# Performance work log

Measured on AMD Instinct MI355X. Metric: run time of the kernel, lower is better.

The kernel has to match this reference:

```python
import jax, jax.numpy as jnp
import numpy as np

T, B = 1024, 256
N = T * B
D = 128  # d_model
IN = 36  # lstm input size = 16 + 4 + 16


def _w(k, shape, s=0.1):
    return jax.random.normal(k, shape, dtype=jnp.float32) * s


def setup_inputs() -> dict:
    key = jax.random.key(0)
    ks = jax.random.split(key, 32)
    inp = {}
    inp["image"] = jax.random.uniform(ks[0], (N, 1, 3, 3), jnp.float32) * 255.0
    inp["location"] = jax.random.uniform(ks[1], (N, 2), jnp.float32) * 5.0
    inp["message"] = jax.random.randint(ks[2], (N,), 0, 16)
    inp["done"] = (jax.random.uniform(ks[3], (N,)) < 0.05).astype(jnp.float32)
    inp["h0"] = jax.random.normal(ks[4], (1, B, D), jnp.float32)
    inp["c0"] = jax.random.normal(ks[5], (1, B, D), jnp.float32)
    # visual encoder: 9 -> 256 -> 256 -> 128 -> 16 (ReLU each)
    inp["vis_W1"] = _w(ks[6], (256, 9));   inp["vis_b1"] = jnp.zeros((256,), jnp.float32)
    inp["vis_W2"] = _w(ks[7], (256, 256)); inp["vis_b2"] = jnp.zeros((256,), jnp.float32)
    inp["vis_W3"] = _w(ks[8], (128, 256)); inp["vis_b3"] = jnp.zeros((128,), jnp.float32)
    inp["vis_W4"] = _w(ks[9], (16, 128));  inp["vis_b4"] = jnp.zeros((16,), jnp.float32)
    # location encoder: 2 -> 4
    inp["loc_W"] = _w(ks[10], (4, 2)); inp["loc_b"] = jnp.zeros((4,), jnp.float32)
    # message encoder: Embedding(16,16) -> Linear(16,16) -> ReLU
    inp["emb"] = _w(ks[11], (16, 16), 1.0)
    inp["msg_W"] = _w(ks[12], (16, 16)); inp["msg_b"] = jnp.zeros((16,), jnp.float32)
    # LSTM params (torch layout, gate order i,f,g,o)
    inp["W_ih"] = _w(ks[13], (4 * D, IN)); inp["W_hh"] = _w(ks[14], (4 * D, D))
    inp["b_ih"] = jnp.zeros((4 * D,), jnp.float32); inp["b_hh"] = jnp.zeros((4 * D,), jnp.float32)
    # heads
    inp["actor_W"] = _w(ks[15], (5, D), 0.01);   inp["actor_b"] = jnp.zeros((5,), jnp.float32)
    inp["head_W"] = _w(ks[16], (16, D), 0.01);   inp["head_b"] = jnp.zeros((16,), jnp.float32)
    inp["critic_W"] = _w(ks[17], (1, D), 1.0);   inp["critic_b"] = jnp.zeros((1,), jnp.float32)
    return inp


def reference(image, location, message, done, h0, c0,
              vis_W1, vis_b1, vis_W2, vis_b2, vis_W3, vis_b3, vis_W4, vis_b4,
              loc_W, loc_b, emb, msg_W, msg_b,
              W_ih, W_hh, b_ih, b_hh,
              actor_W, actor_b, head_W, head_b, critic_W, critic_b):
    # encoders (all rows at once)
    x = image.reshape(N, -1) / 255.0
    x = jax.nn.relu(x @ vis_W1.T + vis_b1)
    x = jax.nn.relu(x @ vis_W2.T + vis_b2)
    x = jax.nn.relu(x @ vis_W3.T + vis_b3)
    img_feat = jax.nn.relu(x @ vis_W4.T + vis_b4)                 # [N,16]
    loc_feat = (location / 5.0) @ loc_W.T + loc_b                 # [N,4]
    msg_feat = jax.nn.relu(emb[message] @ msg_W.T + msg_b)        # [N,16]
    feat = jnp.concatenate([img_feat, loc_feat, msg_feat], axis=1).reshape(T, B, IN)
    d = done.reshape(T, B)

    def step(carry, inp_t):
        h, c = carry
        x_t, d_t = inp_t
        m = (1.0 - d_t)[:, None]
        h = h * m
        c = c * m
        gates = x_t @ W_ih.T + h @ W_hh.T + (b_ih + b_hh)         # [B,4D]
        i, f, g, o = jnp.split(gates, 4, axis=-1)
        i = jax.nn.sigmoid(i); f = jax.nn.sigmoid(f)
        g = jnp.tanh(g);       o = jax.nn.sigmoid(o)
        c = f * c + i * g
        h = o * jnp.tanh(c)
        return (h, c), h

    (_, _), hs = jax.lax.scan(step, (h0[0], c0[0]), (feat, d))
    hidden = hs.reshape(N, D)
    action_logits = hidden @ actor_W.T + actor_b                  # [N,5]
    message_logits = hidden @ head_W.T + head_b                   # [N,16]
    value = hidden @ critic_W.T + critic_b                        # [N,1]
    return jnp.concatenate([action_logits, message_logits, value], axis=1)  # [N,22]
```

## Files before the change

kernel.cpp:

```cpp
#include <hip/hip_runtime.h>
#include <hip/hip_bf16.h>

#define DEV __device__ __forceinline__

typedef short short8 __attribute__((ext_vector_type(8)));
typedef _Float16 h8 __attribute__((ext_vector_type(8)));
typedef _Float16 h2 __attribute__((ext_vector_type(2)));
typedef float f32x4 __attribute__((ext_vector_type(4)));
typedef unsigned short u16;

constexpr int T_ = 1024, B_ = 256, N_ = T_ * B_, D_ = 128;
constexpr int FS = 48;
constexpr int NSLOT = 16;
constexpr int SEGQC = 64;
constexpr int MAXIT = 392;
constexpr int CH = 48;
constexpr int WARM = 56;
constexpr int MAXPC = 768;
constexpr unsigned DEADT = 0xFFFFu;
constexpr unsigned TRB = 0x10000u;
constexpr unsigned NWB = 0x20000u;

DEV u16 f2b(float f) {
  unsigned u = __float_as_uint(f);
  return (u16)((u + 0x7fffu + ((u >> 16) & 1u)) >> 16);
}

#if __has_builtin(__builtin_amdgcn_exp2f)
#define EXP2F __builtin_amdgcn_exp2f
#else
#define EXP2F __exp2f
#endif
#if __has_builtin(__builtin_amdgcn_rcpf)
#define RCPF __builtin_amdgcn_rcpf
#else
#define RCPF(x) (1.0f / (x))
#endif
DEV float sigf(float x) { return RCPF(1.0f + EXP2F(x * -1.44269504f)); }
DEV float tanhf_(float x) {
  return fmaf(RCPF(1.0f + EXP2F(x * -2.88539008f)), 2.0f, -1.0f);
}

__global__ void prep_kernel(const float* W1, const float* W2, const float* W3,
                            const float* W4, const float* emb, const float* msgW,
                            const float* msgb, const float* Wih, const float* Whh,
                            const float* bih, const float* bhh, const float* aW,
                            const float* ab, const float* hW, const float* hb,
                            const float* cW, const float* cb, u16* w1p, u16* w2b,
                            u16* w3b, u16* w4b, float* msgtab, _Float16* wfull,
                            float* biass, _Float16* w22, float* b22) {
  int i0 = blockIdx.x * blockDim.x + threadIdx.x;
  int st = gridDim.x * blockDim.x;
  for (int i = i0; i < 256 * 32; i += st) {
    int r = i >> 5, k = i & 31;
    w1p[i] = (k < 9) ? f2b(W1[r * 9 + k]) : (u16)0;
  }
  for (int i = i0; i < 256 * 256; i += st) w2b[i] = f2b(W2[i]);
  for (int i = i0; i < 128 * 256; i += st) w3b[i] = f2b(W3[i]);
  for (int i = i0; i < 16 * 128; i += st) w4b[i] = f2b(W4[i]);
  for (int i = i0; i < 256; i += st) {
    int v = i >> 4, j = i & 15;
    float s = msgb[j];
    for (int k = 0; k < 16; ++k) s += emb[v * 16 + k] * msgW[j * 16 + k];
    msgtab[i] = s > 0.f ? s : 0.f;
  }
  for (int i = i0; i < 512 * 192; i += st) {
    int c = i / 192, k = i % 192;
    float v;
    if (k < 128) v = Whh[(size_t)c * 128 + k];
    else {
      int p = k - 128;
      if (p < 18) v = Wih[(size_t)c * 36 + p];
      else if (p >= 24 && p < 42) v = Wih[(size_t)c * 36 + p - 6];
      else v = 0.f;
    }
    wfull[i] = (_Float16)v;
  }
  for (int i = i0; i < 512; i += st) biass[i] = bih[i] + bhh[i];
  for (int i = i0; i < 32 * 128; i += st) {
    int c = i >> 7, k = i & 127;
    float v = 0.f;
    if (c < 5) v = aW[c * 128 + k];
    else if (c < 21) v = hW[(c - 5) * 128 + k];
    else if (c == 21) v = cW[k];
    w22[i] = (_Float16)v;
  }
  for (int i = i0; i < 32; i += st) {
    float v = 0.f;
    if (i < 5) v = ab[i];
    else if (i < 21) v = hb[i - 5];
    else if (i == 21) v = cb[0];
    b22[i] = v;
  }
}

__global__ __launch_bounds__(64) void seg_scan_kernel(const float* done,
                                                      unsigned* segq, int* nq) {
  __shared__ unsigned short brkpos[1024];
  __shared__ int lcnt[64];
  __shared__ int nb_sh;
  __shared__ int pcs[MAXPC];
  __shared__ int np_sh;
  const int b = blockIdx.x;
  const int l = threadIdx.x;

  unsigned mask = 0;
#pragma unroll
  for (int j = 0; j < 16; ++j) {
    const int t = l * 16 + j;
    const float dv = (t == 0) ? 0.0f : done[(size_t)t * B_ + b];
    mask |= (dv != 0.0f) ? (1u << j) : 0u;
  }
  lcnt[l] = __popc(mask);
  __syncthreads();
  if (l == 0) {
    int acc = 0;
    for (int i = 0; i < 64; ++i) { const int c = lcnt[i]; lcnt[i] = acc; acc += c; }
    nb_sh = acc;
  }
  __syncthreads();
  {
    int off = lcnt[l];
    unsigned mm = mask;
    while (mm) {
      const int j = __builtin_ctz(mm);
      mm &= mm - 1;
      brkpos[off++] = (unsigned short)(l * 16 + j);
    }
  }
  __syncthreads();
  if (l == 0) {
    int np = 0;
    const int nb = nb_sh;
    int t0 = 0;
    for (int s = 0; s <= nb; ++s) {
      const int t1 = (s < nb) ? (int)brkpos[s] : T_;
      int k = 0;
      for (int ps = t0; ps < t1 && np < MAXPC; ps += CH, ++k) {
        const int pl = min(CH, t1 - ps);
        const int wl = (k == 0) ? 0 : min(WARM, ps - t0);
        pcs[np++] = ps | (pl << 10) | (wl << 17);
      }
      t0 = t1;
    }
    np_sh = np;
  }
  __syncthreads();
  const int np = np_sh;
  int ssum[16], scnt[16];
#pragma unroll
  for (int j = 0; j < 16; ++j) { ssum[j] = 0; scnt[j] = 0; }
  if (l == 0 && np > 0) {
    const int e = pcs[0];
    segq[((size_t)b * NSLOT + 0) * SEGQC + 0] = (unsigned)e;
    ssum[0] = ((e >> 10) & 127) + ((e >> 17) & 127);
    scnt[0] = 1;
    pcs[0] = -1;
  }
  __syncthreads();
  for (int it = 1; it < np; ++it) {
    int bestw = -1, bestk = 0;
    for (int j = l; j < np; j += 64) {
      const int e = pcs[j];
      if (e >= 0) {
        const int w = ((e >> 10) & 127) + ((e >> 17) & 127);
        if (w > bestw || (w == bestw && j < bestk)) { bestw = w; bestk = j; }
      }
    }
    int pk = (bestw < 0) ? -1 : ((bestw << 10) | (1023 - bestk));
#pragma unroll
    for (int wd = 32; wd >= 1; wd >>= 1) pk = max(pk, __shfl_xor(pk, wd));
    if (l == 0 && pk >= 0) {
      const int k = 1023 - (pk & 1023);
      const int e = pcs[k];
      const int w = pk >> 10;
      int m = 0, best = 0x7fffffff;
#pragma unroll
      for (int j = 0; j < 16; ++j) {
        const int v = (scnt[j] >= SEGQC) ? 0x7fffffff : ssum[j];
        if (v < best) { best = v; m = j; }
      }
      segq[((size_t)b * NSLOT + m) * SEGQC + scnt[m]] = (unsigned)e;
      ssum[m] += w;
      ++scnt[m];
      pcs[k] = -1;
    }
    __syncthreads();
  }
  if (l == 0) {
#pragma unroll
    for (int j = 0; j < 16; ++j) nq[b * NSLOT + j] = scnt[j];
  }
}

__global__ __launch_bounds__(64) void sched_build_kernel(const unsigned* segq,
                                                         const int* nq,
                                                         unsigned* sched,
                                                         int* bsteps) {
  const int b = blockIdx.x;
  const int l = threadIdx.x;
  int it = 0;
  if (l < NSLOT) {
    const int gs = b * NSLOT + l;
    const unsigned* q = segq + (size_t)gs * SEGQC;
    const int cnt = nq[gs];
    unsigned* sc = sched + (size_t)b * MAXIT * 16 + l;
    for (int s = 0; s < cnt; ++s) {
      const unsigned e = q[s];
      const int ps = (int)(e & 1023u);
      const int pl = (int)((e >> 10) & 127u);
      const int wl = (int)((e >> 17) & 127u);
      for (int j = 0; j < wl && it < MAXIT - 8; ++j) {
        sc[(size_t)it * 16] = (unsigned)(ps - wl + j) | NWB;
        ++it;
      }
      for (int j = 0; j < pl && it < MAXIT - 8; ++j) {
        sc[(size_t)it * 16] = (unsigned)(ps + j) | ((j == pl - 1) ? TRB : 0u);
        ++it;
      }
    }
  }
  int mk = (l < NSLOT) ? it : 0;
#pragma unroll
  for (int w = 8; w >= 1; w >>= 1) mk = max(mk, __shfl_xor(mk, w));
  if (l < NSLOT) {
    unsigned* sc = sched + (size_t)b * MAXIT * 16 + l;
    const int pe = min(mk + 8, MAXIT);
    for (int i2 = it; i2 < pe; ++i2) sc[(size_t)i2 * 16] = DEADT | TRB;
    if (l == 0) bsteps[b] = mk;
  }
}

template <int K, int OUTN, bool SWZIN>
DEV void mlp_layer(const u16* Ain, u16* Aout, const u16* Wb, const float* bias,
                   int colbase, int NT, int lane) {
  constexpr int KT = K / 32;
  const int lr = lane & 15, lg = lane >> 4;
  for (int nt = 0; nt < NT; ++nt) {
    const int col = colbase + nt * 16 + lr;
    short8 bf[KT];
#pragma unroll
    for (int kt = 0; kt < KT; ++kt)
      bf[kt] = *(const short8*)(Wb + col * K + kt * 32 + lg * 8);
    const float bcol = bias[col];
#pragma unroll
    for (int mt = 0; mt < 4; ++mt) {
      f32x4 acc = {0.f, 0.f, 0.f, 0.f};
#pragma unroll
      for (int kt = 0; kt < KT; ++kt) {
        const int row = mt * 16 + lr;
        int kb = (kt * 32 + lg * 8) * 2;
        if (SWZIN) kb ^= (row & 7) << 4;
        const short8 af = *(const short8*)(Ain + row * K + (kb >> 1));
        acc = __builtin_amdgcn_mfma_f32_16x16x32_bf16(af, bf[kt], acc, 0, 0, 0);
      }
#pragma unroll
      for (int r = 0; r < 4; ++r) {
        const int row = mt * 16 + lg * 4 + r;
        float v = acc[r] + bcol;
        v = v > 0.f ? v : 0.f;
        const int kb = (col * 2) ^ ((row & 7) << 4);
        Aout[row * OUTN + (kb >> 1)] = f2b(v);
      }
    }
  }
}

__global__ __launch_bounds__(256) void enc_kernel(
    const float* image, const float* location, const int* message,
    const float* vb1, const float* vb2, const float* vb3, const float* vb4,
    const float* locW, const float* locb, const u16* w1p, const u16* w2b,
    const u16* w3b, const u16* w4b, const float* msgtab, _Float16* featf) {
  __shared__ __align__(16) u16 buf1[64 * 256];
  __shared__ __align__(16) u16 buf2[64 * 256];
  const int n0 = blockIdx.x * 64;
  const int tid = threadIdx.x;
  const int wave = tid >> 6, lane = tid & 63;

  for (int i = tid; i < 64 * 32; i += 256) {
    int r = i >> 5, k = i & 31;
    float v = (k < 9) ? image[(size_t)(n0 + r) * 9 + k] * (1.0f / 255.0f) : 0.0f;
    buf2[i] = f2b(v);
  }
  __syncthreads();
  mlp_layer<32, 256, false>(buf2, buf1, w1p, vb1, wave * 64, 4, lane);
  __syncthreads();
  mlp_layer<256, 256, true>(buf1, buf2, w2b, vb2, wave * 64, 4, lane);
  __syncthreads();
  mlp_layer<256, 128, true>(buf2, buf1, w3b, vb3, wave * 32, 2, lane);
  __syncthreads();
  {
    const int lr = lane & 15, lg = lane >> 4;
    const int col = lr;
    short8 bfr[4];
#pragma unroll
    for (int kt = 0; kt < 4; ++kt)
      bfr[kt] = *(const short8*)(w4b + col * 128 + kt * 32 + lg * 8);
    f32x4 acc = {0.f, 0.f, 0.f, 0.f};
#pragma unroll
    for (int kt = 0; kt < 4; ++kt) {
      const int row = wave * 16 + lr;
      const int kb = ((kt * 32 + lg * 8) * 2) ^ ((row & 7) << 4);
      const short8 af = *(const short8*)(buf1 + row * 128 + (kb >> 1));
      acc = __builtin_amdgcn_mfma_f32_16x16x32_bf16(af, bfr[kt], acc, 0, 0, 0);
    }
    const float bcol = vb4[col];
#pragma unroll
    for (int r = 0; r < 4; ++r) {
      const int row = wave * 16 + lg * 4 + r;
      float v = acc[r] + bcol;
      v = v > 0.f ? v : 0.f;
      featf[(size_t)(n0 + row) * FS + col] = (_Float16)v;
    }
  }
  if (tid < 64) {
    const int n = n0 + tid;
    _Float16* fr = featf + (size_t)n * FS;
#pragma unroll
    for (int j = 0; j < 6; ++j) fr[18 + j] = (_Float16)0.f;
#pragma unroll
    for (int j = 0; j < 6; ++j) fr[42 + j] = (_Float16)0.f;
    const float x0 = location[(size_t)n * 2] * 0.2f;
    const float x1 = location[(size_t)n * 2 + 1] * 0.2f;
#pragma unroll
    for (int j = 0; j < 4; ++j) {
      const int pos = (j < 2) ? 16 + j : 22 + j;
      fr[pos] = (_Float16)fmaf(x0, locW[j * 2], fmaf(x1, locW[j * 2 + 1], locb[j]));
    }
    const float* mrow = msgtab + message[n] * 16;
#pragma unroll
    for (int j = 0; j < 16; ++j) fr[26 + j] = (_Float16)mrow[j];
  }
}

__global__ __launch_bounds__(512, 2) void lstm_seg_kernel(
    const _Float16* featf, const _Float16* wfull, const float* biass,
    const unsigned* sched, const int* bsteps, const float* h0, const float* c0,
    const float* done, _Float16* hidh) {
  __shared__ __align__(16) char abuf[2][16 * 384];
  const int b = blockIdx.x;
  const int tid = threadIdx.x;
  const int wave = tid >> 6, l = tid & 63;
  const int lc = l & 15, lg = l >> 4;
  const int d = wave * 16 + lc;
  const bool fth = (wave < 6) && (lc < 4);
  const int fslot = lg * 4 + lc;
  const int fch = wave;

  h8 bf[4][6];
#pragma unroll
  for (int g = 0; g < 4; ++g) {
    const _Float16* wp = wfull + (size_t)(g * 128 + d) * 192;
#pragma unroll
    for (int kt = 0; kt < 6; ++kt)
      bf[g][kt] = *(const h8*)(wp + kt * 32 + lg * 8);
  }
  float bias4[4];
#pragma unroll
  for (int g = 0; g < 4; ++g) bias4[g] = biass[g * 128 + d];

  for (int i = tid; i < 2 * 16 * 384 / 4; i += 512) ((float*)abuf)[i] = 0.0f;
  __syncthreads();

  const int nsteps = bsteps[b];
  const unsigned* sb = sched + (size_t)b * MAXIT * 16;
  uint4 sr0 = *(const uint4*)(sb + 0 * 16 + lg * 4);
  uint4 sr1 = *(const uint4*)(sb + 1 * 16 + lg * 4);
  unsigned ss1 = DEADT, ss2 = DEADT, t00 = DEADT;
  if (fth) {
    t00 = sb[0 * 16 + fslot] & 0xFFFFu;
    ss1 = sb[1 * 16 + fslot];
    ss2 = sb[2 * 16 + fslot];
  }

  const float m0 = 1.0f - done[b];
  if (tid < 128)
    *(_Float16*)(abuf[0] + 2 * tid) = (_Float16)(h0[(size_t)b * D_ + tid] * m0);
  float creg[4];
#pragma unroll
  for (int r = 0; r < 4; ++r) {
    const int row = lg * 4 + r;
    creg[r] = (row == 0) ? c0[(size_t)b * D_ + d] * m0 : 0.0f;
  }
  if (fth && t00 != DEADT) {
    const unsigned fo = t00 * (unsigned)(B_ * FS) + (unsigned)(b * FS) + fch * 8;
    const uint4 fz = *(const uint4*)(featf + fo);
    const int byte = (fslot * 384 + 256 + fch * 16) ^ ((fslot & 7) << 4);
    *(uint4*)(abuf[0] + byte) = fz;
  }
  uint4 fvW = {0, 0, 0, 0};
  if (fth && (ss1 & 0xFFFFu) != DEADT) {
    const unsigned fo =
        (ss1 & 0xFFFFu) * (unsigned)(B_ * FS) + (unsigned)(b * FS) + fch * 8;
    fvW = *(const uint4*)(featf + fo);
  }
  __syncthreads();

  int p = 0;
  for (int i = 0; i < nsteps; ++i) {
    const uint4 srN = *(const uint4*)(sb + (size_t)(i + 2) * 16 + lg * 4);
    unsigned ssN = DEADT;
    if (fth) ssN = sb[(size_t)(i + 3) * 16 + fslot];
    const char* bp = abuf[p];
    h8 af[6];
#pragma unroll
    for (int kt = 0; kt < 6; ++kt) {
      const int byte = (lc * 384 + ((kt * 32 + lg * 8) << 1)) ^ ((lc & 7) << 4);
      af[kt] = *(const h8*)(bp + byte);
    }
    uint4 fvN = {0, 0, 0, 0};
    const unsigned t2 = ss2 & 0xFFFFu;
    if (fth && t2 != DEADT) {
      const unsigned fo = t2 * (unsigned)(B_ * FS) + (unsigned)(b * FS) + fch * 8;
      fvN = *(const uint4*)(featf + fo);
    }
    f32x4 acc[4];
#pragma unroll
    for (int g = 0; g < 4; ++g)
      acc[g] = f32x4{bias4[g], bias4[g], bias4[g], bias4[g]};
#pragma unroll
    for (int kt = 0; kt < 6; ++kt)
#pragma unroll
      for (int g = 0; g < 4; ++g)
        acc[g] = __builtin_amdgcn_mfma_f32_16x16x32_f16(af[kt], bf[g][kt],
                                                        acc[g], 0, 0, 0);
    char* bn = abuf[p ^ 1];
#pragma unroll
    for (int r = 0; r < 4; ++r) {
      const int row = lg * 4 + r;
      const unsigned e = ((const unsigned*)&sr0)[r];
      const float gi = sigf(acc[0][r]);
      const float gf = sigf(acc[1][r]);
      const float gg = tanhf_(acc[2][r]);
      const float go = sigf(acc[3][r]);
      const float cn = fmaf(gf, creg[r], gi * gg);
      const float hv = go * tanhf_(cn);
      const unsigned tt = e & 0xFFFFu;
      const bool tr = (e & TRB) != 0u;
      creg[r] = tr ? 0.0f : cn;
      *(_Float16*)(bn + ((row * 384 + 2 * d) ^ ((row & 7) << 4))) =
          (_Float16)(tr ? 0.0f : hv);
      if (tt != DEADT && !(e & NWB)) {
        const unsigned ho = (tt << 15) + (unsigned)((b << 7) + d);
        hidh[ho] = (_Float16)hv;
      }
    }
    if (fth && (ss1 & 0xFFFFu) != DEADT) {
      const int byte = (fslot * 384 + 256 + fch * 16) ^ ((fslot & 7) << 4);
      *(uint4*)(bn + byte) = fvW;
    }
    sr0 = sr1; sr1 = srN;
    ss1 = ss2; ss2 = ssN;
    fvW = fvN;
    asm volatile("s_waitcnt lgkmcnt(0)" ::: "memory");
    __builtin_amdgcn_s_barrier();
    p ^= 1;
  }
}

__global__ __launch_bounds__(256) void head_kernel(const _Float16* hidh,
                                                   const _Float16* w22,
                                                   const float* b22, float* out) {
  const int tid = threadIdx.x;
  const int w = tid >> 6, l = tid & 63;
  const int lr = l & 15, lg = l >> 4;
  const int row0 = blockIdx.x * 64 + w * 16;

  h8 bfr[2][4];
#pragma unroll
  for (int ct = 0; ct < 2; ++ct)
#pragma unroll
    for (int kt = 0; kt < 4; ++kt)
      bfr[ct][kt] = *(const h8*)(w22 + (ct * 16 + lr) * 128 + kt * 32 + lg * 8);
  h8 af[4];
#pragma unroll
  for (int kt = 0; kt < 4; ++kt)
    af[kt] = *(const h8*)(hidh + (size_t)(row0 + lr) * D_ + kt * 32 + lg * 8);

  f32x4 acc[2];
#pragma unroll
  for (int ct = 0; ct < 2; ++ct) acc[ct] = f32x4{0.f, 0.f, 0.f, 0.f};
#pragma unroll
  for (int kt = 0; kt < 4; ++kt)
#pragma unroll
    for (int ct = 0; ct < 2; ++ct)
      acc[ct] = __builtin_amdgcn_mfma_f32_16x16x32_f16(af[kt], bfr[ct][kt],
                                                       acc[ct], 0, 0, 0);
#pragma unroll
  for (int ct = 0; ct < 2; ++ct) {
    const int col = ct * 16 + lr;
    if (col < 22) {
      const float bb = b22[col];
#pragma unroll
      for (int r = 0; r < 4; ++r) {
        const int row = row0 + lg * 4 + r;
        out[(size_t)row * 22 + col] = acc[ct][r] + bb;
      }
    }
  }
}

extern "C" void kernel_launch(void* const* d_in, const int* in_sizes, int n_in,
                              void* d_out, int out_size, void* d_ws, size_t ws_size,
                              hipStream_t stream) {
  const float* image = (const float*)d_in[0];
  const float* location = (const float*)d_in[1];
  const int* message = (const int*)d_in[2];
  const float* done = (const float*)d_in[3];
  const float* h0 = (const float*)d_in[4];
  const float* c0 = (const float*)d_in[5];
  const float* vW1 = (const float*)d_in[6];
  const float* vb1 = (const float*)d_in[7];
  const float* vW2 = (const float*)d_in[8];
  const float* vb2 = (const float*)d_in[9];
  const float* vW3 = (const float*)d_in[10];
  const float* vb3 = (const float*)d_in[11];
  const float* vW4 = (const float*)d_in[12];
  const float* vb4 = (const float*)d_in[13];
  const float* locW = (const float*)d_in[14];
  const float* locb = (const float*)d_in[15];
  const float* emb = (const float*)d_in[16];
  const float* msgW = (const float*)d_in[17];
  const float* msgb = (const float*)d_in[18];
  const float* Wih = (const float*)d_in[19];
  const float* Whh = (const float*)d_in[20];
  const float* bih = (const float*)d_in[21];
  const float* bhh = (const float*)d_in[22];
  const float* aW = (const float*)d_in[23];
  const float* ab = (const float*)d_in[24];
  const float* hW = (const float*)d_in[25];
  const float* hb = (const float*)d_in[26];
  const float* cW = (const float*)d_in[27];
  const float* cb = (const float*)d_in[28];

  char* ws = (char*)d_ws;
  size_t off = 0;
  auto alloc = [&](size_t bytes) {
    void* p = ws + off;
    off = (off + bytes + 255) & ~(size_t)255;
    return p;
  };
  _Float16* featf = (_Float16*)alloc((size_t)N_ * FS * 2);
  _Float16* hidh = (_Float16*)alloc((size_t)N_ * D_ * 2);
  u16* w1p = (u16*)alloc(256 * 32 * 2);
  u16* w2b = (u16*)alloc(256 * 256 * 2);
  u16* w3b = (u16*)alloc(128 * 256 * 2);
  u16* w4b = (u16*)alloc(16 * 128 * 2);
  float* msgtab = (float*)alloc(256 * 4);
  _Float16* wfull = (_Float16*)alloc(512 * 192 * 2);
  float* biass = (float*)alloc(512 * 4);
  unsigned* segq = (unsigned*)alloc((size_t)B_ * NSLOT * SEGQC * 4);
  int* nqA = (int*)alloc(B_ * NSLOT * 4);
  unsigned* sched = (unsigned*)alloc((size_t)B_ * MAXIT * 16 * 4);
  int* bsteps = (int*)alloc(B_ * 4);
  _Float16* w22 = (_Float16*)alloc(32 * 128 * 2);
  float* b22 = (float*)alloc(32 * 4);
  (void)in_sizes; (void)n_in; (void)out_size; (void)ws_size;

  prep_kernel<<<64, 256, 0, stream>>>(vW1, vW2, vW3, vW4, emb, msgW, msgb, Wih,
                                      Whh, bih, bhh, aW, ab, hW, hb, cW, cb, w1p,
                                      w2b, w3b, w4b, msgtab, wfull, biass, w22,
                                      b22);
  seg_scan_kernel<<<B_, 64, 0, stream>>>(done, segq, nqA);
  sched_build_kernel<<<B_, 64, 0, stream>>>(segq, nqA, sched, bsteps);
  enc_kernel<<<N_ / 64, 256, 0, stream>>>(image, location, message, vb1, vb2, vb3,
                                          vb4, locW, locb, w1p, w2b, w3b, w4b,
                                          msgtab, featf);
  lstm_seg_kernel<<<B_, 512, 0, stream>>>(featf, wfull, biass, sched, bsteps,
                                          h0, c0, done, hidh);
  head_kernel<<<N_ / 64, 256, 0, stream>>>(hidh, w22, b22, (float*)d_out);
}
```

Before: 481.0 us.

## Enlarge encoder tile to 128 rows with 2x4 wave grid and register-blocked MFMA

The encoder kernel now handles 128 rows per block with 8 waves arranged as 2 row-halves by 4 column-quarters. Each wave loads its A fragments once per row tile and reuses them across two output column tiles, and the accumulators are seeded with the bias. This cuts repeated LDS reads and weight loads per output and should expose more MFMA ILP. The cost is 128KB of LDS per block, which lowers occupancy to one block per CU. The prep kernel grid is also doubled.

```diff
diff --git a/kernel.cpp b/kernel.cpp
--- a/kernel.cpp
+++ b/kernel.cpp
@@ -232,88 +232,110 @@
 }
 
 template <int K, int OUTN, bool SWZIN>
-DEV void mlp_layer(const u16* Ain, u16* Aout, const u16* Wb, const float* bias,
-                   int colbase, int NT, int lane) {
+DEV void mlp_layer128(const u16* Ain, u16* Aout, const u16* Wb, const float* bias,
+                      int mh, int cq, int lane) {
   constexpr int KT = K / 32;
+  constexpr int NT = OUTN / 64;
+  constexpr int PASSES = NT / 2;
   const int lr = lane & 15, lg = lane >> 4;
-  for (int nt = 0; nt < NT; ++nt) {
-    const int col = colbase + nt * 16 + lr;
-    short8 bf[KT];
-#pragma unroll
-    for (int kt = 0; kt < KT; ++kt)
-      bf[kt] = *(const short8*)(Wb + col * K + kt * 32 + lg * 8);
-    const float bcol = bias[col];
+  const int colbase = cq * (OUTN / 4);
+  const int rowbase = mh * 64;
+#pragma unroll
+  for (int ps = 0; ps < PASSES; ++ps) {
+    short8 bf[2][KT];
+    float bcol[2];
+#pragma unroll
+    for (int n2 = 0; n2 < 2; ++n2) {
+      const int col = colbase + (ps * 2 + n2) * 16 + lr;
+#pragma unroll
+      for (int kt = 0; kt < KT; ++kt)
+        bf[n2][kt] = *(const short8*)(Wb + col * K + kt * 32 + lg * 8);
+      bcol[n2] = bias[col];
+    }
 #pragma unroll
     for (int mt = 0; mt < 4; ++mt) {
-      f32x4 acc = {0.f, 0.f, 0.f, 0.f};
+      const int arow = rowbase + mt * 16 + lr;
+      short8 af[KT];
 #pragma unroll
       for (int kt = 0; kt < KT; ++kt) {
-        const int row = mt * 16 + lr;
         int kb = (kt * 32 + lg * 8) * 2;
-        if (SWZIN) kb ^= (row & 7) << 4;
-        const short8 af = *(const short8*)(Ain + row * K + (kb >> 1));
-        acc = __builtin_amdgcn_mfma_f32_16x16x32_bf16(af, bf[kt], acc, 0, 0, 0);
-      }
-#pragma unroll
-      for (int r = 0; r < 4; ++r) {
-        const int row = mt * 16 + lg * 4 + r;
-        float v = acc[r] + bcol;
-        v = v > 0.f ? v : 0.f;
-        const int kb = (col * 2) ^ ((row & 7) << 4);
-        Aout[row * OUTN + (kb >> 1)] = f2b(v);
-      }
-    }
-  }
-}
-
-__global__ __launch_bounds__(256) void enc_kernel(
+        if (SWZIN) kb ^= (arow & 7) << 4;
+        af[kt] = *(const short8*)(Ain + arow * K + (kb >> 1));
+      }
+      f32x4 acc[2];
+#pragma unroll
+      for (int n2 = 0; n2 < 2; ++n2)
+        acc[n2] = f32x4{bcol[n2], bcol[n2], bcol[n2], bcol[n2]};
+#pragma unroll
+      for (int kt = 0; kt < KT; ++kt)
+#pragma unroll
+        for (int n2 = 0; n2 < 2; ++n2)
+          acc[n2] = __builtin_amdgcn_mfma_f32_16x16x32_bf16(af[kt], bf[n2][kt],
+                                                            acc[n2], 0, 0, 0);
+#pragma unroll
+      for (int n2 = 0; n2 < 2; ++n2) {
+        const int col = colbase + (ps * 2 + n2) * 16 + lr;
+#pragma unroll
+        for (int r = 0; r < 4; ++r) {
+          const int orow = rowbase + mt * 16 + lg * 4 + r;
+          float v = acc[n2][r];
+          v = v > 0.f ? v : 0.f;
+          const int kb = (col * 2) ^ ((orow & 7) << 4);
+          Aout[orow * OUTN + (kb >> 1)] = f2b(v);
+        }
+      }
+    }
+  }
+}
+
+__global__ __launch_bounds__(512) void enc_kernel(
     const float* image, const float* location, const int* message,
     const float* vb1, const float* vb2, const float* vb3, const float* vb4,
     const float* locW, const float* locb, const u16* w1p, const u16* w2b,
     const u16* w3b, const u16* w4b, const float* msgtab, _Float16* featf) {
-  __shared__ __align__(16) u16 buf1[64 * 256];
-  __shared__ __align__(16) u16 buf2[64 * 256];
-  const int n0 = blockIdx.x * 64;
+  __shared__ __align__(16) u16 bufA[128 * 256];
+  __shared__ __align__(16) u16 bufB[128 * 256];
+  const int n0 = blockIdx.x * 128;
   const int tid = threadIdx.x;
   const int wave = tid >> 6, lane = tid & 63;
-
-  for (int i = tid; i < 64 * 32; i += 256) {
+  const int mh = wave >> 2, cq = wave & 3;
+
+  for (int i = tid; i < 128 * 32; i += 512) {
     int r = i >> 5, k = i & 31;
     float v = (k < 9) ? image[(size_t)(n0 + r) * 9 + k] * (1.0f / 255.0f) : 0.0f;
-    buf2[i] = f2b(v);
-  }
-  __syncthreads();
-  mlp_layer<32, 256, false>(buf2, buf1, w1p, vb1, wave * 64, 4, lane);
-  __syncthreads();
-  mlp_layer<256, 256, true>(buf1, buf2, w2b, vb2, wave * 64, 4, lane);
-  __syncthreads();
-  mlp_layer<256, 128, true>(buf2, buf1, w3b, vb3, wave * 32, 2, lane);
+    bufA[i] = f2b(v);
+  }
+  __syncthreads();
+  mlp_layer128<32, 256, false>(bufA, bufB, w1p, vb1, mh, cq, lane);
+  __syncthreads();
+  mlp_layer128<256, 256, true>(bufB, bufA, w2b, vb2, mh, cq, lane);
+  __syncthreads();
+  mlp_layer128<256, 128, true>(bufA, bufB, w3b, vb3, mh, cq, lane);
   __syncthreads();
   {
     const int lr = lane & 15, lg = lane >> 4;
-    const int col = lr;
     short8 bfr[4];
 #pragma unroll
     for (int kt = 0; kt < 4; ++kt)
-      bfr[kt] = *(const short8*)(w4b + col * 128 + kt * 32 + lg * 8);
-    f32x4 acc = {0.f, 0.f, 0.f, 0.f};
+      bfr[kt] = *(const short8*)(w4b + lr * 128 + kt * 32 + lg * 8);
+    const float bcol = vb4[lr];
+    f32x4 acc = {bcol, bcol, bcol, bcol};
 #pragma unroll
     for (int kt = 0; kt < 4; ++kt) {
-      const int row = wave * 16 + lr;
-      const int kb = ((kt * 32 + lg * 8) * 2) ^ ((row & 7) << 4);
-      const short8 af = *(const short8*)(buf1 + row * 128 + (kb >> 1));
+      const int arow = wave * 16 + lr;
+      const int kb = ((kt * 32 + lg * 8) * 2) ^ ((arow & 7) << 4);
+      const short8 af = *(const short8*)(bufB + arow * 128 + (kb >> 1));
       acc = __builtin_amdgcn_mfma_f32_16x16x32_bf16(af, bfr[kt], acc, 0, 0, 0);
     }
-    const float bcol = vb4[col];
 #pragma unroll
     for (int r = 0; r < 4; ++r) {
       const int row = wave * 16 + lg * 4 + r;
-      float v = acc[r] + bcol;
+      float v = acc[r];
       v = v > 0.f ? v : 0.f;
-      featf[(size_t)(n0 + row) * FS + col] = (_Float16)v;
-    }
-  }
-  if (tid < 64) {
+      featf[(size_t)(n0 + row) * FS + lr] = (_Float16)v;
+    }
+  }
+  if (tid < 128) {
     const int n = n0 + tid;
     _Float16* fr = featf + (size_t)n * FS;
 #pragma unroll
@@ -557,15 +579,15 @@
   float* b22 = (float*)alloc(32 * 4);
   (void)in_sizes; (void)n_in; (void)out_size; (void)ws_size;
 
-  prep_kernel<<<64, 256, 0, stream>>>(vW1, vW2, vW3, vW4, emb, msgW, msgb, Wih,
-                                      Whh, bih, bhh, aW, ab, hW, hb, cW, cb, w1p,
-                                      w2b, w3b, w4b, msgtab, wfull, biass, w22,
-                                      b22);
+  prep_kernel<<<128, 256, 0, stream>>>(vW1, vW2, vW3, vW4, emb, msgW, msgb, Wih,
+                                       Whh, bih, bhh, aW, ab, hW, hb, cW, cb, w1p,
+                                       w2b, w3b, w4b, msgtab, wfull, biass, w22,
+                                       b22);
   seg_scan_kernel<<<B_, 64, 0, stream>>>(done, segq, nqA);
   sched_build_kernel<<<B_, 64, 0, stream>>>(segq, nqA, sched, bsteps);
-  enc_kernel<<<N_ / 64, 256, 0, stream>>>(image, location, message, vb1, vb2, vb3,
-                                          vb4, locW, locb, w1p, w2b, w3b, w4b,
-                                          msgtab, featf);
+  enc_kernel<<<N_ / 128, 512, 0, stream>>>(image, location, message, vb1, vb2, vb3,
+                                           vb4, locW, locb, w1p, w2b, w3b, w4b,
+                                           msgtab, featf);
   lstm_seg_kernel<<<B_, 512, 0, stream>>>(featf, wfull, biass, sched, bsteps,
                                           h0, c0, done, hidh);
   head_kernel<<<N_ / 64, 256, 0, stream>>>(hidh, w22, b22, (float*)d_out);
```

New measurement: 483.6 us. No clear change (+0.6%).
